# Kernel tuning notes

Measured on AMD Instinct MI355X. Metric: run time of the kernel, lower is better.

The kernel has to match this reference:

```python
import jax, jax.numpy as jnp
import numpy as np

FOCAL_ALPHA = 0.25
FOCAL_GAMMA = 2.0
LAMBDA_L1, LAMBDA_GIOU, LAMBDA_CONF = 1.0, 2.0, 1.0
IOU_THRESH = 0.3  # hardcoded `max_iou > 0.3` in assign_positives


def _make_boxes(key, shape):
    # valid xyxy boxes in [0,1]: random center + moderate size
    r = jax.random.uniform(key, shape + (4,), dtype=jnp.float32)
    cx = 0.1 + 0.8 * r[..., 0]
    cy = 0.1 + 0.8 * r[..., 1]
    w = 0.05 + 0.30 * r[..., 2]
    h = 0.05 + 0.30 * r[..., 3]
    return jnp.stack([cx - w / 2, cy - h / 2, cx + w / 2, cy + h / 2], axis=-1)


def setup_inputs() -> dict:
    key = jax.random.key(0)
    k1, k2, k3, k4, k5 = jax.random.split(key, 5)
    B, C, H, W, N = 16, 64, 80, 80, 32
    pred_boxes = _make_boxes(k1, (B, C, H, W))          # [B,C,H,W,4] xyxy
    confidences = jax.random.uniform(k2, (B, C, H, W), dtype=jnp.float32)
    cam = jax.random.uniform(k3, (B, C, H, W), dtype=jnp.float32)
    gt_boxes = _make_boxes(k4, (B, N))                   # [B,N,4] xyxy
    gt_labels = jax.random.randint(k5, (B, N), 0, C, dtype=jnp.int32)
    return {"pred_boxes": pred_boxes, "confidences": confidences, "cam": cam,
            "gt_boxes": gt_boxes, "gt_labels": gt_labels}


def box_giou(b1, b2):
    """Generalized IoU for xyxy boxes, broadcasting over leading dims."""
    a1 = (b1[..., 2] - b1[..., 0]) * (b1[..., 3] - b1[..., 1])
    a2 = (b2[..., 2] - b2[..., 0]) * (b2[..., 3] - b2[..., 1])
    lt = jnp.maximum(b1[..., :2], b2[..., :2])
    rb = jnp.minimum(b1[..., 2:], b2[..., 2:])
    wh = jnp.clip(rb - lt, 0.0)
    inter = wh[..., 0] * wh[..., 1]
    union = a1 + a2 - inter
    iou = inter / union
    lte = jnp.minimum(b1[..., :2], b2[..., :2])
    rbe = jnp.maximum(b1[..., 2:], b2[..., 2:])
    whe = jnp.clip(rbe - lte, 0.0)
    ae = whe[..., 0] * whe[..., 1]
    return iou - (ae - union) / ae


def _loss(pred_boxes, confidences, cam, gt_boxes, gt_labels):
    B, C, H, W, _ = pred_boxes.shape
    N = gt_boxes.shape[1]
    ii = jnp.arange(H)
    jj = jnp.arange(W)
    ch = jnp.arange(C)

    def assign_one(pb, gb, gl):  # pb [C,H,W,4], gb [N,4], gl [N]
        def step(carry, g):
            pos, matched = carry
            lab = gl[g]
            box = gb[g]
            pc = pb[lab].reshape(H * W, 4)
            giou = box_giou(pc, box[None, :])          # [H*W]
            idx = jnp.argmax(giou)
            valid = giou[idx] > IOU_THRESH
            mi, mj = idx // W, idx % W
            # pos_radius=1.5 -> window rows [mi-2, mi+1], cols [mj-2, mj+1]
            win = (((ii >= mi - 2) & (ii <= mi + 1))[:, None]
                   & ((jj >= mj - 2) & (jj <= mj + 1))[None, :])
            full = (ch == lab)[:, None, None] & (valid & win)[None]
            return (pos | full, jnp.where(full, g, matched)), None

        init = (jnp.zeros((C, H, W), bool), jnp.full((C, H, W), -1, jnp.int32))
        (pos, matched), _ = jax.lax.scan(step, init, jnp.arange(N))
        return pos, matched

    pos_mask, matched = jax.vmap(assign_one)(pred_boxes, gt_boxes, gt_labels)
    # gather matched gt box per position (later gts overwrite earlier, as in scan)
    gt_at = jax.vmap(lambda gb, m: gb[m])(gt_boxes, jnp.maximum(matched, 0))  # [B,C,H,W,4]

    l1 = jnp.mean(jnp.abs(pred_boxes - gt_at), axis=-1)   # F.l1_loss per pair
    giou_p = box_giou(pred_boxes, gt_at)
    num_pos = jnp.sum(pos_mask)
    denom = jnp.maximum(num_pos, 1).astype(jnp.float32)
    loss_l1 = jnp.sum(jnp.where(pos_mask, l1, 0.0)) / denom
    loss_giou = jnp.sum(jnp.where(pos_mask, 1.0 - giou_p, 0.0)) / denom

    conf_t = pos_mask.astype(jnp.float32)
    p = jnp.clip(confidences, 1e-6, 1.0 - 1e-6)
    ce = -(conf_t * jnp.log(p) + (1.0 - conf_t) * jnp.log1p(-p))
    p_t = p * conf_t + (1.0 - p) * (1.0 - conf_t)
    alpha_t = FOCAL_ALPHA * conf_t + (1.0 - FOCAL_ALPHA) * (1.0 - conf_t)
    loss_conf = jnp.mean(alpha_t * (1.0 - p_t) ** FOCAL_GAMMA * ce)

    loss_total = LAMBDA_L1 * loss_l1 + LAMBDA_GIOU * loss_giou + LAMBDA_CONF * loss_conf
    pos_ratio = num_pos.astype(jnp.float32) / (B * C * H * W)
    return loss_l1, loss_giou, loss_conf, loss_total, pos_ratio


@jax.jit
def reference(pred_boxes, confidences, cam, gt_boxes, gt_labels):
    return _loss(pred_boxes, confidences, cam, gt_boxes, gt_labels)
```

## Files before the change

kernel.cpp:

```cpp
#include <hip/hip_runtime.h>
#include <math.h>

constexpr int B = 16, C = 64, H = 80, Wd = 80, N = 32;
constexpr int HW = H * Wd;
constexpr int CHW = C * HW;
constexpr long long TOTAL = (long long)B * CHW;

constexpr int NCHUNK = 5;
constexpr int CHUNK_ELEMS = HW / NCHUNK;
constexpr int A_DEPTH = CHUNK_ELEMS / 256;


__global__ __launch_bounds__(256) void assign_partial_kernel(
    const float* __restrict__ pred,
    const float* __restrict__ gtb,
    const int*   __restrict__ gtl,
    int2* __restrict__ amax)
{
#pragma clang fp contract(off)
    const int blk = blockIdx.x;
    const int bg = blk / NCHUNK;
    const int chunk = blk - bg * NCHUNK;
    const int b = bg >> 5;
    const int tid = threadIdx.x;

    const int lab = gtl[bg];
    const float4 gb = ((const float4*)gtb)[bg];
    const float a2 = (gb.z - gb.x) * (gb.w - gb.y);

    const float4* pc = (const float4*)(pred + (size_t)(b * C + lab) * HW * 4)
                       + chunk * CHUNK_ELEMS;

    float4 buf[A_DEPTH];
#pragma unroll
    for (int k = 0; k < A_DEPTH; k++)
        buf[k] = pc[tid + k * 256];

    float best = -INFINITY;
    int bidx = 0x7fffffff;
#pragma unroll
    for (int k = 0; k < A_DEPTH; k++) {
        float4 pb = buf[k];
        float a1 = (pb.z - pb.x) * (pb.w - pb.y);
        float ltx = fmaxf(pb.x, gb.x), lty = fmaxf(pb.y, gb.y);
        float rbx = fminf(pb.z, gb.z), rby = fminf(pb.w, gb.w);
        float wx = fmaxf(rbx - ltx, 0.0f), wy = fmaxf(rby - lty, 0.0f);
        float inter = wx * wy;
        float uni = (a1 + a2) - inter;
        float iou = inter / uni;
        float lex = fminf(pb.x, gb.x), ley = fminf(pb.y, gb.y);
        float rex = fmaxf(pb.z, gb.z), rey = fmaxf(pb.w, gb.w);
        float ex = fmaxf(rex - lex, 0.0f), ey = fmaxf(rey - ley, 0.0f);
        float ae = ex * ey;
        float gi = iou - (ae - uni) / ae;
        if (gi > best) { best = gi; bidx = chunk * CHUNK_ELEMS + tid + k * 256; }
    }

#pragma unroll
    for (int off = 32; off > 0; off >>= 1) {
        float ov = __shfl_down(best, off, 64);
        int   oi = __shfl_down(bidx, off, 64);
        if (ov > best || (ov == best && oi < bidx)) { best = ov; bidx = oi; }
    }

    __shared__ float sv[4];
    __shared__ int   si[4];
    if ((tid & 63) == 0) { sv[tid >> 6] = best; si[tid >> 6] = bidx; }
    __syncthreads();
    if (tid == 0) {
        float bv = sv[0]; int bi = si[0];
#pragma unroll
        for (int wv = 1; wv < 4; wv++) {
            if (sv[wv] > bv || (sv[wv] == bv && si[wv] < bi)) {
                bv = sv[wv]; bi = si[wv];
            }
        }
        amax[blk] = make_int2(__float_as_int(bv), bi);
    }
}

constexpr int K2_PER_THREAD = 16;
constexpr int K2_BLOCK_ELEMS = 256 * K2_PER_THREAD;
constexpr int K2_BLOCKS_PER_BATCH = CHW / K2_BLOCK_ELEMS;
constexpr int NBLK = B * K2_BLOCKS_PER_BATCH;

__global__ __launch_bounds__(256) void main_kernel(
    const float* __restrict__ pred,
    const float* __restrict__ conf,
    const float* __restrict__ gtb,
    const int*   __restrict__ gtl,
    const int2*  __restrict__ amax,
    float4* __restrict__ partials)
{
    const int tid = threadIdx.x;
    const int b = blockIdx.x / K2_BLOCKS_PER_BATCH;
    const int base = (blockIdx.x % K2_BLOCKS_PER_BATCH) * K2_BLOCK_ELEMS;
    const int pos0 = base + tid * K2_PER_THREAD;

    const float4* conf4 = (const float4*)(conf + (size_t)b * CHW);
    float4 q[4];
#pragma unroll
    for (int k = 0; k < 4; k++) q[k] = conf4[(pos0 >> 2) + k];

    const int c = pos0 / HW;
    const int rem = pos0 - c * HW;
    const int h = rem / Wd;
    const int w0 = rem - h * Wd;

    __shared__ int s_cnt;
    __shared__ int4 s_gt[N];
    if (tid == 0) s_cnt = 0;
    __syncthreads();
    const int c0 = base / HW;
    const int c1 = (base + K2_BLOCK_ELEMS - 1) / HW;
    if (tid < N) {
        const int bg = b * N + tid;
        float best = -INFINITY;
        int idx = 0x7fffffff;
#pragma unroll
        for (int kc = 0; kc < NCHUNK; kc++) {
            int2 pr = amax[bg * NCHUNK + kc];
            float v = __int_as_float(pr.x);
            if (v > best || (v == best && pr.y < idx)) { best = v; idx = pr.y; }
        }
        if (best > 0.3f) {
            int lab = gtl[bg];
            if (lab >= c0 && lab <= c1) {
                int k = atomicAdd(&s_cnt, 1);
                s_gt[k] = make_int4(tid, lab, idx / Wd, idx % Wd);
            }
        }
    }
    __syncthreads();
    const int cnt = s_cnt;

    float pv[K2_PER_THREAD];
#pragma unroll
    for (int k = 0; k < 4; k++) {
        pv[4 * k + 0] = q[k].x; pv[4 * k + 1] = q[k].y;
        pv[4 * k + 2] = q[k].z; pv[4 * k + 3] = q[k].w;
    }

    float l_f = 0.0f;
#pragma unroll
    for (int e = 0; e < K2_PER_THREAD; e++) {
        float p = fminf(fmaxf(pv[e], 1e-6f), 1.0f - 1e-6f);
        l_f += 0.75f * p * p * (-__logf(1.0f - p));
    }

    float l_l1 = 0.0f, l_gi = 0.0f, l_np = 0.0f;
    if (cnt) {
        int m[K2_PER_THREAD];
#pragma unroll
        for (int e = 0; e < K2_PER_THREAD; e++) m[e] = -1;
        for (int j = 0; j < cnt; j++) {
            int4 a = s_gt[j];
            if (a.y == c && h >= a.z - 2 && h <= a.z + 1) {
#pragma unroll
                for (int e = 0; e < K2_PER_THREAD; e++) {
                    int w = w0 + e;
                    if (w >= a.w - 2 && w <= a.w + 1) m[e] = max(m[e], a.x);
                }
            }
        }
#pragma unroll
        for (int e = 0; e < K2_PER_THREAD; e++) {
            if (m[e] >= 0) {
#pragma clang fp contract(off)
                float p = fminf(fmaxf(pv[e], 1e-6f), 1.0f - 1e-6f);
                float om = 1.0f - p;
                l_f += 0.25f * om * om * (-__logf(p))
                     - 0.75f * p * p * (-__logf(1.0f - p));
                l_np += 1.0f;

                int pos = pos0 + e;
                float4 pb = *(const float4*)(pred + ((size_t)b * CHW + pos) * 4);
                float4 gb = ((const float4*)gtb)[b * N + m[e]];
                l_l1 += 0.25f * (fabsf(pb.x - gb.x) + fabsf(pb.y - gb.y) +
                                 fabsf(pb.z - gb.z) + fabsf(pb.w - gb.w));

                float a1 = (pb.z - pb.x) * (pb.w - pb.y);
                float a2 = (gb.z - gb.x) * (gb.w - gb.y);
                float ltx = fmaxf(pb.x, gb.x), lty = fmaxf(pb.y, gb.y);
                float rbx = fminf(pb.z, gb.z), rby = fminf(pb.w, gb.w);
                float wx = fmaxf(rbx - ltx, 0.0f), wy = fmaxf(rby - lty, 0.0f);
                float inter = wx * wy;
                float uni = (a1 + a2) - inter;
                float iou = inter / uni;
                float lex = fminf(pb.x, gb.x), ley = fminf(pb.y, gb.y);
                float rex = fmaxf(pb.z, gb.z), rey = fmaxf(pb.w, gb.w);
                float ex = fmaxf(rex - lex, 0.0f), ey = fmaxf(rey - ley, 0.0f);
                float ae = ex * ey;
                float gi = iou - (ae - uni) / ae;
                l_gi += 1.0f - gi;
            }
        }
    }

#pragma unroll
    for (int off = 32; off > 0; off >>= 1) {
        l_l1 += __shfl_down(l_l1, off, 64);
        l_gi += __shfl_down(l_gi, off, 64);
        l_f  += __shfl_down(l_f,  off, 64);
        l_np += __shfl_down(l_np, off, 64);
    }
    __shared__ float4 swv[4];
    if ((tid & 63) == 0) swv[tid >> 6] = make_float4(l_l1, l_gi, l_f, l_np);
    __syncthreads();
    if (tid == 0) {
        float4 s = swv[0];
#pragma unroll
        for (int wv = 1; wv < 4; wv++) {
            s.x += swv[wv].x; s.y += swv[wv].y;
            s.z += swv[wv].z; s.w += swv[wv].w;
        }
        partials[blockIdx.x] = s;
    }
}

__global__ __launch_bounds__(256) void final_kernel(
    const float4* __restrict__ partials,
    float* __restrict__ out)
{
    const int tid = threadIdx.x;
    float s0 = 0.0f, s1 = 0.0f, s2 = 0.0f, s3 = 0.0f;
    for (int i = tid; i < NBLK; i += 256) {
        float4 p = partials[i];
        s0 += p.x; s1 += p.y; s2 += p.z; s3 += p.w;
    }
#pragma unroll
    for (int off = 32; off > 0; off >>= 1) {
        s0 += __shfl_down(s0, off, 64);
        s1 += __shfl_down(s1, off, 64);
        s2 += __shfl_down(s2, off, 64);
        s3 += __shfl_down(s3, off, 64);
    }
    __shared__ float4 swv[4];
    if ((tid & 63) == 0) swv[tid >> 6] = make_float4(s0, s1, s2, s3);
    __syncthreads();
    if (tid == 0) {
        float4 s = swv[0];
#pragma unroll
        for (int wv = 1; wv < 4; wv++) {
            s.x += swv[wv].x; s.y += swv[wv].y;
            s.z += swv[wv].z; s.w += swv[wv].w;
        }
        float np = s.w;
        float denom = fmaxf(np, 1.0f);
        float l1 = s.x / denom;
        float gi = s.y / denom;
        float cf = s.z / (float)TOTAL;
        out[0] = l1;
        out[1] = gi;
        out[2] = cf;
        out[3] = l1 + 2.0f * gi + cf;
        out[4] = np / (float)TOTAL;
    }
}

extern "C" void kernel_launch(void* const* d_in, const int* in_sizes, int n_in,
                              void* d_out, int out_size, void* d_ws, size_t ws_size,
                              hipStream_t stream) {
    const float* pred = (const float*)d_in[0];
    const float* conf = (const float*)d_in[1];
    const float* gtb  = (const float*)d_in[3];
    const int*   gtl  = (const int*)d_in[4];

    int2*   amax     = (int2*)d_ws;
    float4* partials = (float4*)((char*)d_ws + 32768);
    float*  out      = (float*)d_out;

    assign_partial_kernel<<<B * N * NCHUNK, 256, 0, stream>>>(pred, gtb, gtl, amax);
    main_kernel<<<NBLK, 256, 0, stream>>>(pred, conf, gtb, gtl, amax, partials);
    final_kernel<<<1, 256, 0, stream>>>(partials, out);
}
```

Before: 188.1 us.

## Fuse assignment with negative focal pass and handle positives sparsely per GT

The assignment argmax blocks and the dense negative-focal sum over confidences now run in one launch. The positive-cell corrections (focal delta, L1, GIoU) are then computed sparsely: one wave per GT covers its 4x4 neighbourhood and resolves duplicates against later GTs. The final reduction is folded into the second kernel through a last-block atomic counter. This removes a full dense pass over confidences that scanned the GT list, plus one kernel launch, at the cost of threadfence/atomic ordering and duplicate-resolution logic.

```diff
diff --git a/kernel.cpp b/kernel.cpp
--- a/kernel.cpp
+++ b/kernel.cpp
@@ -9,190 +9,206 @@
 constexpr int NCHUNK = 5;
 constexpr int CHUNK_ELEMS = HW / NCHUNK;
 constexpr int A_DEPTH = CHUNK_ELEMS / 256;
-
-
-__global__ __launch_bounds__(256) void assign_partial_kernel(
-    const float* __restrict__ pred,
-    const float* __restrict__ gtb,
-    const int*   __restrict__ gtl,
-    int2* __restrict__ amax)
-{
-#pragma clang fp contract(off)
-    const int blk = blockIdx.x;
-    const int bg = blk / NCHUNK;
-    const int chunk = blk - bg * NCHUNK;
-    const int b = bg >> 5;
-    const int tid = threadIdx.x;
-
-    const int lab = gtl[bg];
-    const float4 gb = ((const float4*)gtb)[bg];
-    const float a2 = (gb.z - gb.x) * (gb.w - gb.y);
-
-    const float4* pc = (const float4*)(pred + (size_t)(b * C + lab) * HW * 4)
-                       + chunk * CHUNK_ELEMS;
-
-    float4 buf[A_DEPTH];
-#pragma unroll
-    for (int k = 0; k < A_DEPTH; k++)
-        buf[k] = pc[tid + k * 256];
-
-    float best = -INFINITY;
-    int bidx = 0x7fffffff;
-#pragma unroll
-    for (int k = 0; k < A_DEPTH; k++) {
-        float4 pb = buf[k];
-        float a1 = (pb.z - pb.x) * (pb.w - pb.y);
-        float ltx = fmaxf(pb.x, gb.x), lty = fmaxf(pb.y, gb.y);
-        float rbx = fminf(pb.z, gb.z), rby = fminf(pb.w, gb.w);
-        float wx = fmaxf(rbx - ltx, 0.0f), wy = fmaxf(rby - lty, 0.0f);
-        float inter = wx * wy;
-        float uni = (a1 + a2) - inter;
-        float iou = inter / uni;
-        float lex = fminf(pb.x, gb.x), ley = fminf(pb.y, gb.y);
-        float rex = fmaxf(pb.z, gb.z), rey = fmaxf(pb.w, gb.w);
-        float ex = fmaxf(rex - lex, 0.0f), ey = fmaxf(rey - ley, 0.0f);
-        float ae = ex * ey;
-        float gi = iou - (ae - uni) / ae;
-        if (gi > best) { best = gi; bidx = chunk * CHUNK_ELEMS + tid + k * 256; }
-    }
-
-#pragma unroll
-    for (int off = 32; off > 0; off >>= 1) {
-        float ov = __shfl_down(best, off, 64);
-        int   oi = __shfl_down(bidx, off, 64);
-        if (ov > best || (ov == best && oi < bidx)) { best = ov; bidx = oi; }
-    }
-
-    __shared__ float sv[4];
-    __shared__ int   si[4];
-    if ((tid & 63) == 0) { sv[tid >> 6] = best; si[tid >> 6] = bidx; }
-    __syncthreads();
-    if (tid == 0) {
-        float bv = sv[0]; int bi = si[0];
-#pragma unroll
-        for (int wv = 1; wv < 4; wv++) {
-            if (sv[wv] > bv || (sv[wv] == bv && si[wv] < bi)) {
-                bv = sv[wv]; bi = si[wv];
-            }
-        }
-        amax[blk] = make_int2(__float_as_int(bv), bi);
-    }
-}
+constexpr int NBLK_A = B * N * NCHUNK;
 
 constexpr int K2_PER_THREAD = 16;
 constexpr int K2_BLOCK_ELEMS = 256 * K2_PER_THREAD;
 constexpr int K2_BLOCKS_PER_BATCH = CHW / K2_BLOCK_ELEMS;
-constexpr int NBLK = B * K2_BLOCKS_PER_BATCH;
-
-__global__ __launch_bounds__(256) void main_kernel(
+constexpr int NBLK_D = B * K2_BLOCKS_PER_BATCH;
+
+constexpr int NBLK_C = B * N / 4;
+
+#define WS_FOCALP 24576
+#define WS_POSP   32768
+#define WS_DONE   40960
+
+__global__ __launch_bounds__(256) void fused_k1(
+    const float* __restrict__ pred,
+    const float* __restrict__ conf,
+    const float* __restrict__ gtb,
+    const int*   __restrict__ gtl,
+    int2*  __restrict__ amax,
+    float* __restrict__ focalp,
+    int*   __restrict__ done)
+{
+    const int tid = threadIdx.x;
+
+    if (blockIdx.x == 0 && tid == 0) *done = 0;
+
+    if (blockIdx.x < NBLK_A) {
+#pragma clang fp contract(off)
+        const int blk = blockIdx.x;
+        const int bg = blk / NCHUNK;
+        const int chunk = blk - bg * NCHUNK;
+        const int b = bg >> 5;
+
+        const int lab = gtl[bg];
+        const float4 gb = ((const float4*)gtb)[bg];
+        const float a2 = (gb.z - gb.x) * (gb.w - gb.y);
+
+        const float4* pc = (const float4*)(pred + (size_t)(b * C + lab) * HW * 4)
+                           + chunk * CHUNK_ELEMS;
+
+        float4 buf[A_DEPTH];
+#pragma unroll
+        for (int k = 0; k < A_DEPTH; k++)
+            buf[k] = pc[tid + k * 256];
+
+        float best = -INFINITY;
+        int bidx = 0x7fffffff;
+#pragma unroll
+        for (int k = 0; k < A_DEPTH; k++) {
+            float4 pb = buf[k];
+            float a1 = (pb.z - pb.x) * (pb.w - pb.y);
+            float ltx = fmaxf(pb.x, gb.x), lty = fmaxf(pb.y, gb.y);
+            float rbx = fminf(pb.z, gb.z), rby = fminf(pb.w, gb.w);
+            float wx = fmaxf(rbx - ltx, 0.0f), wy = fmaxf(rby - lty, 0.0f);
+            float inter = wx * wy;
+            float uni = (a1 + a2) - inter;
+            float iou = inter / uni;
+            float lex = fminf(pb.x, gb.x), ley = fminf(pb.y, gb.y);
+            float rex = fmaxf(pb.z, gb.z), rey = fmaxf(pb.w, gb.w);
+            float ex = fmaxf(rex - lex, 0.0f), ey = fmaxf(rey - ley, 0.0f);
+            float ae = ex * ey;
+            float gi = iou - (ae - uni) / ae;
+            if (gi > best) { best = gi; bidx = chunk * CHUNK_ELEMS + tid + k * 256; }
+        }
+
+#pragma unroll
+        for (int off = 32; off > 0; off >>= 1) {
+            float ov = __shfl_down(best, off, 64);
+            int   oi = __shfl_down(bidx, off, 64);
+            if (ov > best || (ov == best && oi < bidx)) { best = ov; bidx = oi; }
+        }
+        __shared__ float sv[4];
+        __shared__ int   si[4];
+        if ((tid & 63) == 0) { sv[tid >> 6] = best; si[tid >> 6] = bidx; }
+        __syncthreads();
+        if (tid == 0) {
+            float bv = sv[0]; int bi = si[0];
+#pragma unroll
+            for (int wv = 1; wv < 4; wv++) {
+                if (sv[wv] > bv || (sv[wv] == bv && si[wv] < bi)) {
+                    bv = sv[wv]; bi = si[wv];
+                }
+            }
+            amax[blk] = make_int2(__float_as_int(bv), bi);
+        }
+    } else {
+        const int d = blockIdx.x - NBLK_A;
+        const int b = d / K2_BLOCKS_PER_BATCH;
+        const int base = (d % K2_BLOCKS_PER_BATCH) * K2_BLOCK_ELEMS;
+        const int pos0 = base + tid * K2_PER_THREAD;
+
+        const float4* conf4 = (const float4*)(conf + (size_t)b * CHW);
+        float4 q[4];
+#pragma unroll
+        for (int k = 0; k < 4; k++) q[k] = conf4[(pos0 >> 2) + k];
+
+        float l_f = 0.0f;
+#pragma unroll
+        for (int k = 0; k < 4; k++) {
+            float pv[4] = {q[k].x, q[k].y, q[k].z, q[k].w};
+#pragma unroll
+            for (int e = 0; e < 4; e++) {
+                float p = fminf(fmaxf(pv[e], 1e-6f), 1.0f - 1e-6f);
+                l_f += 0.75f * p * p * (-__logf(1.0f - p));
+            }
+        }
+
+#pragma unroll
+        for (int off = 32; off > 0; off >>= 1)
+            l_f += __shfl_down(l_f, off, 64);
+        __shared__ float swf[4];
+        if ((tid & 63) == 0) swf[tid >> 6] = l_f;
+        __syncthreads();
+        if (tid == 0)
+            focalp[d] = swf[0] + swf[1] + swf[2] + swf[3];
+    }
+}
+
+__global__ __launch_bounds__(256) void fused_k2(
     const float* __restrict__ pred,
     const float* __restrict__ conf,
     const float* __restrict__ gtb,
     const int*   __restrict__ gtl,
     const int2*  __restrict__ amax,
-    float4* __restrict__ partials)
+    const float* __restrict__ focalp,
+    float4* __restrict__ posp,
+    int*    __restrict__ done,
+    float*  __restrict__ out)
 {
     const int tid = threadIdx.x;
-    const int b = blockIdx.x / K2_BLOCKS_PER_BATCH;
-    const int base = (blockIdx.x % K2_BLOCKS_PER_BATCH) * K2_BLOCK_ELEMS;
-    const int pos0 = base + tid * K2_PER_THREAD;
-
-    const float4* conf4 = (const float4*)(conf + (size_t)b * CHW);
-    float4 q[4];
-#pragma unroll
-    for (int k = 0; k < 4; k++) q[k] = conf4[(pos0 >> 2) + k];
-
-    const int c = pos0 / HW;
-    const int rem = pos0 - c * HW;
-    const int h = rem / Wd;
-    const int w0 = rem - h * Wd;
-
-    __shared__ int s_cnt;
-    __shared__ int4 s_gt[N];
-    if (tid == 0) s_cnt = 0;
+    const int b = (blockIdx.x * 4) >> 5;
+
+    __shared__ int2   s_amax[N * NCHUNK];
+    __shared__ int4   s_fin[N];
+    __shared__ float4 s_gtb[N];
+
+    if (tid < N * NCHUNK) s_amax[tid] = amax[b * N * NCHUNK + tid];
+    if (tid < N) s_gtb[tid] = ((const float4*)gtb)[b * N + tid];
     __syncthreads();
-    const int c0 = base / HW;
-    const int c1 = (base + K2_BLOCK_ELEMS - 1) / HW;
+
     if (tid < N) {
-        const int bg = b * N + tid;
         float best = -INFINITY;
         int idx = 0x7fffffff;
 #pragma unroll
         for (int kc = 0; kc < NCHUNK; kc++) {
-            int2 pr = amax[bg * NCHUNK + kc];
+            int2 pr = s_amax[tid * NCHUNK + kc];
             float v = __int_as_float(pr.x);
             if (v > best || (v == best && pr.y < idx)) { best = v; idx = pr.y; }
         }
-        if (best > 0.3f) {
-            int lab = gtl[bg];
-            if (lab >= c0 && lab <= c1) {
-                int k = atomicAdd(&s_cnt, 1);
-                s_gt[k] = make_int4(tid, lab, idx / Wd, idx % Wd);
-            }
-        }
+        int lab = gtl[b * N + tid];
+        s_fin[tid] = make_int4(best > 0.3f ? 1 : 0, idx / Wd, idx % Wd, lab);
     }
     __syncthreads();
-    const int cnt = s_cnt;
-
-    float pv[K2_PER_THREAD];
-#pragma unroll
-    for (int k = 0; k < 4; k++) {
-        pv[4 * k + 0] = q[k].x; pv[4 * k + 1] = q[k].y;
-        pv[4 * k + 2] = q[k].z; pv[4 * k + 3] = q[k].w;
-    }
-
-    float l_f = 0.0f;
-#pragma unroll
-    for (int e = 0; e < K2_PER_THREAD; e++) {
-        float p = fminf(fmaxf(pv[e], 1e-6f), 1.0f - 1e-6f);
-        l_f += 0.75f * p * p * (-__logf(1.0f - p));
-    }
-
-    float l_l1 = 0.0f, l_gi = 0.0f, l_np = 0.0f;
-    if (cnt) {
-        int m[K2_PER_THREAD];
-#pragma unroll
-        for (int e = 0; e < K2_PER_THREAD; e++) m[e] = -1;
-        for (int j = 0; j < cnt; j++) {
-            int4 a = s_gt[j];
-            if (a.y == c && h >= a.z - 2 && h <= a.z + 1) {
-#pragma unroll
-                for (int e = 0; e < K2_PER_THREAD; e++) {
-                    int w = w0 + e;
-                    if (w >= a.w - 2 && w <= a.w + 1) m[e] = max(m[e], a.x);
-                }
-            }
-        }
-#pragma unroll
-        for (int e = 0; e < K2_PER_THREAD; e++) {
-            if (m[e] >= 0) {
+
+    const int g = (blockIdx.x * 4 + (tid >> 6)) & 31;
+    const int lane = tid & 63;
+
+    float l_l1 = 0.0f, l_gi = 0.0f, l_fc = 0.0f, l_np = 0.0f;
+    int4 fin = s_fin[g];
+    if (fin.x && lane < 16) {
+        const int mi = fin.y, mj = fin.z, lab = fin.w;
+        const int r  = mi - 2 + (lane >> 2);
+        const int cc = mj - 2 + (lane & 3);
+        if (r >= 0 && r < H && cc >= 0 && cc < Wd) {
+            bool mine = true;
+            for (int gp = g + 1; gp < N; gp++) {
+                int4 f2 = s_fin[gp];
+                if (f2.x && f2.w == lab &&
+                    r >= f2.y - 2 && r <= f2.y + 1 &&
+                    cc >= f2.z - 2 && cc <= f2.z + 1) { mine = false; break; }
+            }
+            if (mine) {
 #pragma clang fp contract(off)
-                float p = fminf(fmaxf(pv[e], 1e-6f), 1.0f - 1e-6f);
+                const size_t pos = (size_t)b * CHW + (size_t)lab * HW + r * Wd + cc;
+                float p = conf[pos];
+                p = fminf(fmaxf(p, 1e-6f), 1.0f - 1e-6f);
                 float om = 1.0f - p;
-                l_f += 0.25f * om * om * (-__logf(p))
+                l_fc = 0.25f * om * om * (-__logf(p))
                      - 0.75f * p * p * (-__logf(1.0f - p));
-                l_np += 1.0f;
-
-                int pos = pos0 + e;
-                float4 pb = *(const float4*)(pred + ((size_t)b * CHW + pos) * 4);
-                float4 gb = ((const float4*)gtb)[b * N + m[e]];
-                l_l1 += 0.25f * (fabsf(pb.x - gb.x) + fabsf(pb.y - gb.y) +
-                                 fabsf(pb.z - gb.z) + fabsf(pb.w - gb.w));
+                l_np = 1.0f;
+
+                float4 pb = *(const float4*)(pred + pos * 4);
+                float4 gbx = s_gtb[g];
+                l_l1 = 0.25f * (fabsf(pb.x - gbx.x) + fabsf(pb.y - gbx.y) +
+                                fabsf(pb.z - gbx.z) + fabsf(pb.w - gbx.w));
 
                 float a1 = (pb.z - pb.x) * (pb.w - pb.y);
-                float a2 = (gb.z - gb.x) * (gb.w - gb.y);
-                float ltx = fmaxf(pb.x, gb.x), lty = fmaxf(pb.y, gb.y);
-                float rbx = fminf(pb.z, gb.z), rby = fminf(pb.w, gb.w);
+                float a2 = (gbx.z - gbx.x) * (gbx.w - gbx.y);
+                float ltx = fmaxf(pb.x, gbx.x), lty = fmaxf(pb.y, gbx.y);
+                float rbx = fminf(pb.z, gbx.z), rby = fminf(pb.w, gbx.w);
                 float wx = fmaxf(rbx - ltx, 0.0f), wy = fmaxf(rby - lty, 0.0f);
                 float inter = wx * wy;
                 float uni = (a1 + a2) - inter;
                 float iou = inter / uni;
-                float lex = fminf(pb.x, gb.x), ley = fminf(pb.y, gb.y);
-                float rex = fmaxf(pb.z, gb.z), rey = fmaxf(pb.w, gb.w);
+                float lex = fminf(pb.x, gbx.x), ley = fminf(pb.y, gbx.y);
+                float rex = fmaxf(pb.z, gbx.z), rey = fmaxf(pb.w, gbx.w);
                 float ex = fmaxf(rex - lex, 0.0f), ey = fmaxf(rey - ley, 0.0f);
                 float ae = ex * ey;
                 float gi = iou - (ae - uni) / ae;
-                l_gi += 1.0f - gi;
+                l_gi = 1.0f - gi;
             }
         }
     }
@@ -201,12 +217,14 @@
     for (int off = 32; off > 0; off >>= 1) {
         l_l1 += __shfl_down(l_l1, off, 64);
         l_gi += __shfl_down(l_gi, off, 64);
-        l_f  += __shfl_down(l_f,  off, 64);
+        l_fc += __shfl_down(l_fc, off, 64);
         l_np += __shfl_down(l_np, off, 64);
     }
     __shared__ float4 swv[4];
-    if ((tid & 63) == 0) swv[tid >> 6] = make_float4(l_l1, l_gi, l_f, l_np);
+    if ((tid & 63) == 0) swv[tid >> 6] = make_float4(l_l1, l_gi, l_fc, l_np);
     __syncthreads();
+
+    __shared__ bool s_last;
     if (tid == 0) {
         float4 s = swv[0];
 #pragma unroll
@@ -214,47 +232,50 @@
             s.x += swv[wv].x; s.y += swv[wv].y;
             s.z += swv[wv].z; s.w += swv[wv].w;
         }
-        partials[blockIdx.x] = s;
-    }
-}
-
-__global__ __launch_bounds__(256) void final_kernel(
-    const float4* __restrict__ partials,
-    float* __restrict__ out)
-{
-    const int tid = threadIdx.x;
-    float s0 = 0.0f, s1 = 0.0f, s2 = 0.0f, s3 = 0.0f;
-    for (int i = tid; i < NBLK; i += 256) {
-        float4 p = partials[i];
-        s0 += p.x; s1 += p.y; s2 += p.z; s3 += p.w;
-    }
-#pragma unroll
-    for (int off = 32; off > 0; off >>= 1) {
-        s0 += __shfl_down(s0, off, 64);
-        s1 += __shfl_down(s1, off, 64);
-        s2 += __shfl_down(s2, off, 64);
-        s3 += __shfl_down(s3, off, 64);
-    }
-    __shared__ float4 swv[4];
-    if ((tid & 63) == 0) swv[tid >> 6] = make_float4(s0, s1, s2, s3);
+        posp[blockIdx.x] = s;
+        __threadfence();
+        int prev = atomicAdd(done, 1);
+        s_last = (prev == NBLK_C - 1);
+    }
     __syncthreads();
-    if (tid == 0) {
-        float4 s = swv[0];
-#pragma unroll
-        for (int wv = 1; wv < 4; wv++) {
-            s.x += swv[wv].x; s.y += swv[wv].y;
-            s.z += swv[wv].z; s.w += swv[wv].w;
-        }
-        float np = s.w;
-        float denom = fmaxf(np, 1.0f);
-        float l1 = s.x / denom;
-        float gi = s.y / denom;
-        float cf = s.z / (float)TOTAL;
-        out[0] = l1;
-        out[1] = gi;
-        out[2] = cf;
-        out[3] = l1 + 2.0f * gi + cf;
-        out[4] = np / (float)TOTAL;
+
+    if (s_last) {
+        __threadfence();
+        float s0 = 0.0f, s1 = 0.0f, s2 = 0.0f, s3 = 0.0f;
+        for (int i = tid; i < NBLK_D; i += 256)
+            s2 += focalp[i];
+        if (tid < NBLK_C) {
+            float4 p = posp[tid];
+            s0 += p.x; s1 += p.y; s2 += p.z; s3 += p.w;
+        }
+#pragma unroll
+        for (int off = 32; off > 0; off >>= 1) {
+            s0 += __shfl_down(s0, off, 64);
+            s1 += __shfl_down(s1, off, 64);
+            s2 += __shfl_down(s2, off, 64);
+            s3 += __shfl_down(s3, off, 64);
+        }
+        __shared__ float4 fwv[4];
+        if ((tid & 63) == 0) fwv[tid >> 6] = make_float4(s0, s1, s2, s3);
+        __syncthreads();
+        if (tid == 0) {
+            float4 s = fwv[0];
+#pragma unroll
+            for (int wv = 1; wv < 4; wv++) {
+                s.x += fwv[wv].x; s.y += fwv[wv].y;
+                s.z += fwv[wv].z; s.w += fwv[wv].w;
+            }
+            float np = s.w;
+            float denom = fmaxf(np, 1.0f);
+            float l1 = s.x / denom;
+            float gi = s.y / denom;
+            float cf = s.z / (float)TOTAL;
+            out[0] = l1;
+            out[1] = gi;
+            out[2] = cf;
+            out[3] = l1 + 2.0f * gi + cf;
+            out[4] = np / (float)TOTAL;
+        }
     }
 }
 
@@ -266,11 +287,14 @@
     const float* gtb  = (const float*)d_in[3];
     const int*   gtl  = (const int*)d_in[4];
 
-    int2*   amax     = (int2*)d_ws;
-    float4* partials = (float4*)((char*)d_ws + 32768);
-    float*  out      = (float*)d_out;
-
-    assign_partial_kernel<<<B * N * NCHUNK, 256, 0, stream>>>(pred, gtb, gtl, amax);
-    main_kernel<<<NBLK, 256, 0, stream>>>(pred, conf, gtb, gtl, amax, partials);
-    final_kernel<<<1, 256, 0, stream>>>(partials, out);
+    int2*   amax   = (int2*)d_ws;
+    float*  focalp = (float*)((char*)d_ws + WS_FOCALP);
+    float4* posp   = (float4*)((char*)d_ws + WS_POSP);
+    int*    done   = (int*)((char*)d_ws + WS_DONE);
+    float*  out    = (float*)d_out;
+
+    fused_k1<<<NBLK_A + NBLK_D, 256, 0, stream>>>(pred, conf, gtb, gtl,
+                                                  amax, focalp, done);
+    fused_k2<<<NBLK_C, 256, 0, stream>>>(pred, conf, gtb, gtl, amax,
+                                         focalp, posp, done, out);
 }
```

Result: no change. 189.6 us (+0.8%).
